# Kernel optimization log

Measured on AMD Instinct MI355X. Metric: run time of the kernel, lower is better.

## Reference

```python
import jax, jax.numpy as jnp
import numpy as np

B, C, H, W = 2, 4, 32, 256   # batch, num_classes (class 0 = background), range-image H x W
N = H * W                    # candidate points per (batch, class)
RADIUS = 3.0
KM_ITERS = 1
COORD_SCALE = 60.0           # spread lidar x/y so radius-3 NMS is non-trivial


def setup_inputs() -> dict:
    key = jax.random.key(0)
    k1, k2 = jax.random.split(key)
    segmented_channels = jax.random.normal(k1, (B, C, H, W), dtype=jnp.float32)
    lidar = jax.random.normal(k2, (B, 2, H, W), dtype=jnp.float32) * COORD_SCALE
    return {"segmented_channels": segmented_channels, "lidar": lidar}


def _radius_nms(points, mask, radius):
    # Greedy radius NMS in index order: keep point i iff no earlier kept point
    # lies within `radius`. Masked-out points are never kept (keep init = mask).
    n = points.shape[0]
    idx = jnp.arange(n)
    r2 = radius * radius

    def step(keep, i):
        d2 = jnp.sum((points - points[i]) ** 2, axis=-1)       # [N]
        suppress = keep & (d2 < r2) & (idx > i) & keep[i]
        return keep & ~suppress, None

    keep, _ = jax.lax.scan(step, mask, idx)
    return keep


def _kmeans(points, mask, keep, iters):
    # Centers initialized at the NMS-kept points (same index space as points).
    # Each valid class point is assigned to nearest valid center; centers move
    # to the mean of their assigned points.
    n = points.shape[0]
    centers = points
    w = mask.astype(points.dtype)
    BIG = jnp.asarray(1e30, points.dtype)
    for _ in range(iters):
        d2 = jnp.sum((points[:, None, :] - centers[None, :, :]) ** 2, axis=-1)  # [N,N]
        d2 = jnp.where(keep[None, :], d2, BIG)
        assign = jnp.argmin(d2, axis=1)                         # [N]
        sums = jax.ops.segment_sum(points * w[:, None], assign, num_segments=n)
        cnt = jax.ops.segment_sum(w, assign, num_segments=n)
        upd = sums / jnp.maximum(cnt, 1.0)[:, None]
        centers = jnp.where((keep & (cnt > 0))[:, None], upd, centers)
    return centers * keep[:, None].astype(points.dtype)


def reference(segmented_channels, lidar):
    ind = jnp.argmax(segmented_channels, axis=1)                # [B,H,W] class id per cell
    pts = jnp.stack([lidar[:, 0], lidar[:, 1]], axis=-1).reshape(B, N, 2)
    # boolean class masks for foreground classes 1..C-1
    cls_mask = jnp.stack([ind == c for c in range(1, C)], axis=1).reshape(B, C - 1, N)
    pts_all = jnp.broadcast_to(pts[:, None], (B, C - 1, N, 2)).reshape(B * (C - 1), N, 2)
    mask_all = cls_mask.reshape(B * (C - 1), N)

    def per_bc(args):
        p, m = args
        keep = _radius_nms(p, m, RADIUS)
        centers = _kmeans(p, m, keep, KM_ITERS)
        return centers, keep

    centers, keep = jax.lax.map(per_bc, (pts_all, mask_all))
    # centers: padded [B, C-1, N, 2]; keep marks which rows are real detections
    return centers.reshape(B, C - 1, N, 2), keep.reshape(B, C - 1, N)
```

## Files before the change

kernel.cpp:

```cpp
#include <hip/hip_runtime.h>

#define NPTS 8192
#define BCLS 4
#define NP   6
#define R2   9.0f
#define RAD  3.0f
#define GRD  64
#define NCELL (GRD*GRD)
#define LDSK 2048

#define ST_U 0u
#define ST_A 1u
#define ST_D 2u

__global__ __launch_bounds__(1024) void k_fused(
    const float* __restrict__ seg, const float* __restrict__ lidar,
    float* __restrict__ sumx, float* __restrict__ sumy, float* __restrict__ cntw,
    float* __restrict__ out)
{
    const int p = blockIdx.x;
    const int b = p / 3, cls = p % 3 + 1;
    const int tid = threadIdx.x, lane = tid & 63, wv = tid >> 6;
    const int base = p * NPTS;

    __shared__ float2 sps[NPTS];
    __shared__ unsigned int cmb[NPTS];
    __shared__ unsigned int cellpack[NCELL];
    __shared__ unsigned short stk[8][1024];
    __shared__ float ksx[LDSK], ksy[LDSK], kcn[LDSK];
    __shared__ unsigned long long ballots[128];
    __shared__ unsigned int base128[128];
    __shared__ unsigned int wtot[16];
    __shared__ float redbuf[4][16];
    __shared__ float sbminx, sbminy, scell;
    __shared__ int sM, sK;

    volatile unsigned int* vcmb = (volatile unsigned int*)cmb;
    float* ok = out + (size_t)2 * NP * NPTS + base;

    for (int k = tid; k < NPTS; k += 1024) { cmb[k] = ST_U; ok[k] = 0.f; }
    {
        float2* oc = (float2*)(out + (size_t)2 * base);
        for (int k = tid; k < NPTS; k += 1024) oc[k] = make_float2(0.f, 0.f);
    }
    for (int k = tid; k < NCELL; k += 1024) cellpack[k] = 0u;
    for (int k = tid; k < LDSK; k += 1024) { ksx[k] = 0.f; ksy[k] = 0.f; kcn[k] = 0.f; }

    const float* segb = seg + (size_t)b * BCLS * NPTS;
    const float* lx = lidar + (size_t)b * 2 * NPTS;
    const float* ly = lx + NPTS;
    for (int c0 = 0; c0 < 8; ++c0) {
        int n = c0 * 1024 + tid;
        float bv = segb[n];
        int bc = 0;
        #pragma unroll
        for (int c2 = 1; c2 < BCLS; ++c2) {
            float v = segb[c2 * NPTS + n];
            if (v > bv) { bv = v; bc = c2; }
        }
        unsigned long long bal = __ballot(bc == cls);
        if (lane == 0) ballots[c0 * 16 + wv] = bal;
    }
    for (int n = tid; n < NPTS; n += 1024) sps[n] = make_float2(lx[n], ly[n]);
    __syncthreads();
    if (wv == 0) {
        unsigned int s = (unsigned int)__popcll(ballots[2 * lane]) +
                         (unsigned int)__popcll(ballots[2 * lane + 1]);
        for (int d = 1; d < 64; d <<= 1) s += __shfl_xor(s, d, 64);
        if (lane == 0) sM = (int)s;
    }

    const unsigned long long mw = ballots[tid >> 3];
    {
        float mnx = 3e38f, mxx = -3e38f, mny = 3e38f, mxy = -3e38f;
        #pragma unroll
        for (int q = 0; q < 8; ++q) {
            int n = tid * 8 + q;
            bool m = (mw >> (((tid & 7) << 3) + q)) & 1ull;
            float2 c = sps[n];
            if (m) {
                mnx = fminf(mnx, c.x); mxx = fmaxf(mxx, c.x);
                mny = fminf(mny, c.y); mxy = fmaxf(mxy, c.y);
            }
        }
        for (int d = 32; d; d >>= 1) {
            mnx = fminf(mnx, __shfl_xor(mnx, d, 64));
            mxx = fmaxf(mxx, __shfl_xor(mxx, d, 64));
            mny = fminf(mny, __shfl_xor(mny, d, 64));
            mxy = fmaxf(mxy, __shfl_xor(mxy, d, 64));
        }
        if (lane == 0) { redbuf[0][wv] = mnx; redbuf[1][wv] = mxx;
                         redbuf[2][wv] = mny; redbuf[3][wv] = mxy; }
    }
    __syncthreads();
    if (tid == 0) {
        float a = redbuf[0][0], b2 = redbuf[1][0], c = redbuf[2][0], d = redbuf[3][0];
        for (int q = 1; q < 16; ++q) {
            a = fminf(a, redbuf[0][q]); b2 = fmaxf(b2, redbuf[1][q]);
            c = fminf(c, redbuf[2][q]); d = fmaxf(d, redbuf[3][q]);
        }
        sbminx = a; sbminy = c;
        scell = fmaxf(2.0f * RAD, fmaxf(b2 - a, d - c) / 63.0f);
    }
    __syncthreads();
    const float bminx = sbminx, bminy = sbminy, inv = 1.0f / scell;
    const int M = sM;

    float xq[8], yq[8];
    int cellq[8];
    #pragma unroll
    for (int q = 0; q < 8; ++q) {
        int n = tid * 8 + q;
        bool m = (mw >> (((tid & 7) << 3) + q)) & 1ull;
        float2 c = sps[n];
        xq[q] = c.x; yq[q] = c.y;
        int ix = min(GRD - 1, max(0, (int)((c.x - bminx) * inv)));
        int iy = min(GRD - 1, max(0, (int)((c.y - bminy) * inv)));
        cellq[q] = m ? (iy * GRD + ix) : -1;
        if (m) atomicAdd(&cellpack[iy * GRD + ix], 1u);
    }
    __syncthreads();
    {
        unsigned int c4[4], t4 = 0;
        #pragma unroll
        for (int q = 0; q < 4; ++q) { c4[q] = cellpack[tid * 4 + q]; t4 += c4[q]; }
        unsigned int v = t4;
        for (int d = 1; d < 64; d <<= 1) {
            unsigned int u = __shfl_up(v, d, 64);
            if (lane >= d) v += u;
        }
        if (lane == 63) wtot[wv] = v;
        __syncthreads();
        if (tid == 0) {
            unsigned int acc = 0;
            for (int q = 0; q < 16; ++q) { unsigned int t = wtot[q]; wtot[q] = acc; acc += t; }
        }
        __syncthreads();
        unsigned int excl = wtot[wv] + v - t4;
        #pragma unroll
        for (int q = 0; q < 4; ++q) { cellpack[tid * 4 + q] = excl << 16; excl += c4[q]; }
    }
    __syncthreads();
    #pragma unroll
    for (int q = 0; q < 8; ++q) {
        if (cellq[q] >= 0) {
            unsigned int old = atomicAdd(&cellpack[cellq[q]], 1u);
            unsigned int pos = (old >> 16) + (old & 0xffffu);
            sps[pos] = make_float2(xq[q], yq[q]);
            cmb[pos] = ((unsigned int)(tid * 8 + q) << 2) | ST_U;
        }
    }
    __syncthreads();

    #define ROW_DFS(CY, CX0, CX1, NI, ME, DEAD, FU)                               \
    {                                                                             \
        unsigned int wa = cellpack[(CY) * GRD + (CX0)];                           \
        unsigned int wb = cellpack[(CY) * GRD + (CX1)];                           \
        unsigned int f0 = wa >> 16, f1 = (wb >> 16) + (wb & 0xffffu);             \
        for (unsigned int f = f0; f < f1; ++f) {                                  \
            unsigned int wf = vcmb[f];                                            \
            float2 q = sps[f];                                                    \
            float dx = __fsub_rn((ME).x, q.x), dy = __fsub_rn((ME).y, q.y);       \
            float d2 = __fadd_rn(__fmul_rn(dx, dx), __fmul_rn(dy, dy));           \
            bool in = (d2 < R2) & ((int)(wf >> 2) < (NI));                        \
            DEAD |= in & ((wf & 3u) == ST_A);                                     \
            if (in & ((wf & 3u) == ST_U) & ((FU) < 0)) FU = (int)f;               \
        }                                                                         \
    }
    #define SCAN_DFS(NI, ME, DEAD, FU)                                            \
    {                                                                             \
        int cx0 = max(0, (int)(((ME).x - RAD - bminx) * inv));                    \
        int cx1 = min(GRD - 1, (int)(((ME).x + RAD - bminx) * inv));              \
        int cy0 = max(0, (int)(((ME).y - RAD - bminy) * inv));                    \
        int cy1 = min(GRD - 1, (int)(((ME).y + RAD - bminy) * inv));              \
        DEAD = false; FU = -1;                                                    \
        ROW_DFS(cy0, cx0, cx1, NI, ME, DEAD, FU);                                 \
        if (cy1 > cy0) ROW_DFS(cy1, cx0, cx1, NI, ME, DEAD, FU);                  \
    }

    for (int e0 = tid; e0 < M; e0 += 1024) {
        if ((vcmb[e0] & 3u) != ST_U) continue;
        int top = 0;
        stk[0][tid] = (unsigned short)e0;
        while (top >= 0) {
            int e = stk[top][tid];
            unsigned int w = vcmb[e];
            if ((w & 3u) != ST_U) { --top; continue; }
            int ni = (int)(w >> 2);
            float2 me = sps[e];
            bool dead; int fu;
            SCAN_DFS(ni, me, dead, fu);
            if (dead)        { cmb[e] = ((unsigned int)ni << 2) | ST_D; --top; }
            else if (fu < 0) { cmb[e] = ((unsigned int)ni << 2) | ST_A; --top; }
            else if (top < 7)  stk[++top][tid] = (unsigned short)fu;
            else {
                int ec = fu;
                for (;;) {
                    unsigned int wc = vcmb[ec];
                    if ((wc & 3u) != ST_U) break;
                    int nc = (int)(wc >> 2);
                    float2 mc = sps[ec];
                    bool dd; int fc;
                    SCAN_DFS(nc, mc, dd, fc);
                    if (dd)        { cmb[ec] = ((unsigned int)nc << 2) | ST_D; break; }
                    else if (fc < 0){ cmb[ec] = ((unsigned int)nc << 2) | ST_A; break; }
                    ec = fc;
                }
            }
        }
    }
    for (;;) {
        bool any = false;
        for (int e = tid; e < M; e += 1024) {
            unsigned int w = cmb[e];
            if ((w & 3u) != ST_U) continue;
            int ni = (int)(w >> 2);
            float2 me = sps[e];
            bool dead; int fu;
            SCAN_DFS(ni, me, dead, fu);
            if (dead)        cmb[e] = ((unsigned int)ni << 2) | ST_D;
            else if (fu < 0) cmb[e] = ((unsigned int)ni << 2) | ST_A;
            else any = true;
        }
        if (__syncthreads_count(any) == 0) break;
    }

    for (int k = 0; k < 8; ++k) {
        int e = (k << 10) + tid;
        unsigned long long bal = __ballot((cmb[e] & 3u) == ST_A);
        if (lane == 0) ballots[(k << 4) + wv] = bal;
    }
    __syncthreads();
    if (wv == 0) {
        unsigned int p0 = (unsigned int)__popcll(ballots[2 * lane]);
        unsigned int p1 = (unsigned int)__popcll(ballots[2 * lane + 1]);
        unsigned int s = p0 + p1, v = s;
        for (int d = 1; d < 64; d <<= 1) {
            unsigned int u = __shfl_up(v, d, 64);
            if (lane >= d) v += u;
        }
        base128[2 * lane] = v - s;
        base128[2 * lane + 1] = v - p1;
        if (lane == 63) sK = (int)v;
    }
    __syncthreads();
    #define KRANK(E) ((int)base128[(E) >> 6] +                                    \
                      __popcll(ballots[(E) >> 6] & ((1ull << ((E) & 63)) - 1ull)))
    if (sK > LDSK) {
        for (int k = tid; k < NPTS; k += 1024) {
            sumx[base + k] = 0.f; sumy[base + k] = 0.f; cntw[base + k] = 0.f;
        }
        __syncthreads();
    }

    #define ROW_ARGMIN(CY, CX0, CX1, ME, BD, BE, BN)                              \
    {                                                                             \
        unsigned int wa = cellpack[(CY) * GRD + (CX0)];                           \
        unsigned int wb = cellpack[(CY) * GRD + (CX1)];                           \
        unsigned int f0 = wa >> 16, f1 = (wb >> 16) + (wb & 0xffffu);             \
        for (unsigned int f = f0; f < f1; ++f) {                                  \
            unsigned int wf = cmb[f];                                             \
            float2 q = sps[f];                                                    \
            float dx = __fsub_rn((ME).x, q.x), dy = __fsub_rn((ME).y, q.y);       \
            float d2 = __fadd_rn(__fmul_rn(dx, dx), __fmul_rn(dy, dy));           \
            int nf = (int)(wf >> 2);                                              \
            bool better = ((wf & 3u) == ST_A) &                                   \
                          ((d2 < BD) | ((d2 == BD) & (nf < BN)));                 \
            BD = better ? d2 : BD;                                                \
            BE = better ? (int)f : BE;                                            \
            BN = better ? nf : BN;                                                \
        }                                                                         \
    }
    for (int e = tid; e < M; e += 1024) {
        unsigned int w = cmb[e];
        float2 me = sps[e];
        int be;
        if ((w & 3u) == ST_A) {
            be = e;
        } else {
            int cx0 = max(0, (int)((me.x - RAD - bminx) * inv));
            int cx1 = min(GRD - 1, (int)((me.x + RAD - bminx) * inv));
            int cy0 = max(0, (int)((me.y - RAD - bminy) * inv));
            int cy1 = min(GRD - 1, (int)((me.y + RAD - bminy) * inv));
            float bd = 3e38f;
            be = -1;
            int bn = 1 << 30;
            ROW_ARGMIN(cy0, cx0, cx1, me, bd, be, bn);
            if (cy1 > cy0) ROW_ARGMIN(cy1, cx0, cx1, me, bd, be, bn);
            if (be < 0) continue;
        }
        int r = KRANK(be);
        if (r < LDSK) {
            atomicAdd(&ksx[r], me.x);
            atomicAdd(&ksy[r], me.y);
            atomicAdd(&kcn[r], 1.0f);
        } else {
            atomicAdd(&sumx[base + be], me.x);
            atomicAdd(&sumy[base + be], me.y);
            atomicAdd(&cntw[base + be], 1.0f);
        }
    }
    __syncthreads();

    for (int e = tid; e < M; e += 1024) {
        unsigned int w = cmb[e];
        if ((w & 3u) != ST_A) continue;
        int n = (int)(w >> 2);
        int r = KRANK(e);
        float sx, sy, c;
        if (r < LDSK) { sx = ksx[r]; sy = ksy[r]; c = kcn[r]; }
        else { sx = sumx[base + e]; sy = sumy[base + e]; c = cntw[base + e]; }
        out[2 * (base + n)]     = sx / c;
        out[2 * (base + n) + 1] = sy / c;
        ok[n] = 1.0f;
    }
}

extern "C" void kernel_launch(void* const* d_in, const int* in_sizes, int n_in,
                              void* d_out, int out_size, void* d_ws, size_t ws_size,
                              hipStream_t stream) {
    const float* seg   = (const float*)d_in[0];
    const float* lidar = (const float*)d_in[1];
    float* out = (float*)d_out;

    const size_t A = (size_t)NP * NPTS;
    float* sumx = (float*)d_ws;
    float* sumy = sumx + A;
    float* cntw = sumy + A;

    k_fused<<<NP, 1024, 0, stream>>>(seg, lidar, sumx, sumy, cntw, out);
}
```

Measured before the change: 121.3 us.

## Replace per-thread DFS NMS resolution with compacted worklist rounds

Replaces the per-thread depth-first stack resolution of greedy radius NMS with a synchronous round-based scheme. Each round scans only the still-undecided points, held in a compacted LDS worklist built with wave ballots and one atomic per wave, and falls back to full sweeps if the list overflows. This removes volatile LDS reads and divergent per-thread DFS chains. The cost is a block-wide barrier per round and possibly many rounds when dependency chains are long.

After: 108.0 us, median of 2. -11.0%, faster.

```diff
diff --git a/kernel.cpp b/kernel.cpp
--- a/kernel.cpp
+++ b/kernel.cpp
@@ -7,6 +7,7 @@
 #define RAD  3.0f
 #define GRD  64
 #define NCELL (GRD*GRD)
+#define PCAP 2048
 #define LDSK 2048
 
 #define ST_U 0u
@@ -26,8 +27,9 @@
     __shared__ float2 sps[NPTS];
     __shared__ unsigned int cmb[NPTS];
     __shared__ unsigned int cellpack[NCELL];
-    __shared__ unsigned short stk[8][1024];
+    __shared__ unsigned short plist[2][PCAP];
     __shared__ float ksx[LDSK], ksy[LDSK], kcn[LDSK];
+    __shared__ int pcnt[2];
     __shared__ unsigned long long ballots[128];
     __shared__ unsigned int base128[128];
     __shared__ unsigned int wtot[16];
@@ -35,7 +37,6 @@
     __shared__ float sbminx, sbminy, scell;
     __shared__ int sM, sK;
 
-    volatile unsigned int* vcmb = (volatile unsigned int*)cmb;
     float* ok = out + (size_t)2 * NP * NPTS + base;
 
     for (int k = tid; k < NPTS; k += 1024) { cmb[k] = ST_U; ok[k] = 0.f; }
@@ -45,6 +46,7 @@
     }
     for (int k = tid; k < NCELL; k += 1024) cellpack[k] = 0u;
     for (int k = tid; k < LDSK; k += 1024) { ksx[k] = 0.f; ksy[k] = 0.f; kcn[k] = 0.f; }
+    if (tid == 0) { pcnt[0] = 0; pcnt[1] = 0; }
 
     const float* segb = seg + (size_t)b * BCLS * NPTS;
     const float* lx = lidar + (size_t)b * 2 * NPTS;
@@ -152,78 +154,105 @@
     }
     __syncthreads();
 
-    #define ROW_DFS(CY, CX0, CX1, NI, ME, DEAD, FU)                               \
+    #define ROW_FLAGS(CY, CX0, CX1, NI, ME, DEAD, UNDEC)                          \
     {                                                                             \
         unsigned int wa = cellpack[(CY) * GRD + (CX0)];                           \
         unsigned int wb = cellpack[(CY) * GRD + (CX1)];                           \
         unsigned int f0 = wa >> 16, f1 = (wb >> 16) + (wb & 0xffffu);             \
         for (unsigned int f = f0; f < f1; ++f) {                                  \
-            unsigned int wf = vcmb[f];                                            \
+            unsigned int wf = cmb[f];                                             \
             float2 q = sps[f];                                                    \
             float dx = __fsub_rn((ME).x, q.x), dy = __fsub_rn((ME).y, q.y);       \
             float d2 = __fadd_rn(__fmul_rn(dx, dx), __fmul_rn(dy, dy));           \
             bool in = (d2 < R2) & ((int)(wf >> 2) < (NI));                        \
-            DEAD |= in & ((wf & 3u) == ST_A);                                     \
-            if (in & ((wf & 3u) == ST_U) & ((FU) < 0)) FU = (int)f;               \
+            DEAD  |= in & ((wf & 3u) == ST_A);                                    \
+            UNDEC |= in & ((wf & 3u) == ST_U);                                    \
         }                                                                         \
     }
-    #define SCAN_DFS(NI, ME, DEAD, FU)                                            \
+    #define SCAN_FLAGS(NI, ME, DEAD, UNDEC)                                       \
     {                                                                             \
         int cx0 = max(0, (int)(((ME).x - RAD - bminx) * inv));                    \
         int cx1 = min(GRD - 1, (int)(((ME).x + RAD - bminx) * inv));              \
         int cy0 = max(0, (int)(((ME).y - RAD - bminy) * inv));                    \
         int cy1 = min(GRD - 1, (int)(((ME).y + RAD - bminy) * inv));              \
-        DEAD = false; FU = -1;                                                    \
-        ROW_DFS(cy0, cx0, cx1, NI, ME, DEAD, FU);                                 \
-        if (cy1 > cy0) ROW_DFS(cy1, cx0, cx1, NI, ME, DEAD, FU);                  \
-    }
-
-    for (int e0 = tid; e0 < M; e0 += 1024) {
-        if ((vcmb[e0] & 3u) != ST_U) continue;
-        int top = 0;
-        stk[0][tid] = (unsigned short)e0;
-        while (top >= 0) {
-            int e = stk[top][tid];
-            unsigned int w = vcmb[e];
-            if ((w & 3u) != ST_U) { --top; continue; }
+        DEAD = false; UNDEC = false;                                              \
+        ROW_FLAGS(cy0, cx0, cx1, NI, ME, DEAD, UNDEC);                            \
+        if (cy1 > cy0) ROW_FLAGS(cy1, cx0, cx1, NI, ME, DEAD, UNDEC);             \
+    }
+
+    for (int e = tid; e < M; e += 1024) {
+        unsigned int w = cmb[e];
+        int ni = (int)(w >> 2);
+        float2 me = sps[e];
+        bool dead, undec;
+        SCAN_FLAGS(ni, me, dead, undec);
+        if (dead) cmb[e] = (w & ~3u) | ST_D;
+        else if (!undec) cmb[e] = (w & ~3u) | ST_A;
+        bool pendf = !dead && undec;
+        unsigned long long act = __ballot(true);
+        unsigned long long bal = __ballot(pendf);
+        int leader = __builtin_ctzll(act);
+        int cnt = __popcll(bal);
+        int wbase = 0;
+        if (lane == leader && cnt) wbase = atomicAdd(&pcnt[0], cnt);
+        wbase = __shfl(wbase, leader, 64);
+        if (pendf) {
+            int pos = wbase + __popcll(bal & ((1ull << lane) - 1ull));
+            if (pos < PCAP) plist[0][pos] = (unsigned short)e;
+        }
+    }
+
+    int cur = 0;
+    for (int round = 0; round < NPTS; ++round) {
+        __syncthreads();
+        int pc = pcnt[cur];
+        if (pc == 0) break;
+        if (pc > PCAP) {
+            for (;;) {
+                bool any = false;
+                __syncthreads();
+                for (int e = tid; e < M; e += 1024) {
+                    unsigned int w = cmb[e];
+                    if ((w & 3u) != ST_U) continue;
+                    int ni = (int)(w >> 2);
+                    float2 me = sps[e];
+                    bool dead, undec;
+                    SCAN_FLAGS(ni, me, dead, undec);
+                    if (dead) cmb[e] = (w & ~3u) | ST_D;
+                    else if (!undec) cmb[e] = (w & ~3u) | ST_A;
+                    else any = true;
+                }
+                if (__syncthreads_count(any) == 0) break;
+            }
+            break;
+        }
+        if (tid == 0) pcnt[cur ^ 1] = 0;
+        __syncthreads();
+        for (int idx = tid; idx < pc; idx += 1024) {
+            int e = plist[cur][idx];
+            unsigned int w = cmb[e];
             int ni = (int)(w >> 2);
             float2 me = sps[e];
-            bool dead; int fu;
-            SCAN_DFS(ni, me, dead, fu);
-            if (dead)        { cmb[e] = ((unsigned int)ni << 2) | ST_D; --top; }
-            else if (fu < 0) { cmb[e] = ((unsigned int)ni << 2) | ST_A; --top; }
-            else if (top < 7)  stk[++top][tid] = (unsigned short)fu;
-            else {
-                int ec = fu;
-                for (;;) {
-                    unsigned int wc = vcmb[ec];
-                    if ((wc & 3u) != ST_U) break;
-                    int nc = (int)(wc >> 2);
-                    float2 mc = sps[ec];
-                    bool dd; int fc;
-                    SCAN_DFS(nc, mc, dd, fc);
-                    if (dd)        { cmb[ec] = ((unsigned int)nc << 2) | ST_D; break; }
-                    else if (fc < 0){ cmb[ec] = ((unsigned int)nc << 2) | ST_A; break; }
-                    ec = fc;
-                }
+            bool dead, undec;
+            SCAN_FLAGS(ni, me, dead, undec);
+            if (dead) cmb[e] = (w & ~3u) | ST_D;
+            else if (!undec) cmb[e] = (w & ~3u) | ST_A;
+            bool pendf = !dead && undec;
+            unsigned long long act = __ballot(true);
+            unsigned long long bal = __ballot(pendf);
+            int leader = __builtin_ctzll(act);
+            int cnt = __popcll(bal);
+            int wbase = 0;
+            if (lane == leader && cnt) wbase = atomicAdd(&pcnt[cur ^ 1], cnt);
+            wbase = __shfl(wbase, leader, 64);
+            if (pendf) {
+                int pos = wbase + __popcll(bal & ((1ull << lane) - 1ull));
+                if (pos < PCAP) plist[cur ^ 1][pos] = (unsigned short)e;
             }
         }
-    }
-    for (;;) {
-        bool any = false;
-        for (int e = tid; e < M; e += 1024) {
-            unsigned int w = cmb[e];
-            if ((w & 3u) != ST_U) continue;
-            int ni = (int)(w >> 2);
-            float2 me = sps[e];
-            bool dead; int fu;
-            SCAN_DFS(ni, me, dead, fu);
-            if (dead)        cmb[e] = ((unsigned int)ni << 2) | ST_D;
-            else if (fu < 0) cmb[e] = ((unsigned int)ni << 2) | ST_A;
-            else any = true;
-        }
-        if (__syncthreads_count(any) == 0) break;
-    }
+        cur ^= 1;
+    }
+    __syncthreads();
 
     for (int k = 0; k < 8; ++k) {
         int e = (k << 10) + tid;
```
